# Kernel optimization log

Measured on AMD Instinct MI355X. Metric: run time of the kernel, lower is better.

## Reference

```python
import jax, jax.numpy as jnp
import numpy as np

N_NODES = 100000
N_EDGES = 1600000
N_GRAPHS = 1024
DIM_IN = 128
DIM_SELF = 16
BN_EPS = 1e-5


def _bn(x, gamma, beta):
    # training-mode BatchNorm1d over dim 0 (biased variance, as torch uses for normalization)
    m = jnp.mean(x, axis=0)
    v = jnp.mean((x - m) ** 2, axis=0)
    return gamma * (x - m) * jax.lax.rsqrt(v + BN_EPS) + beta


def _mlp(x, W1, b1, g, b, W2, b2):
    h = x @ W1 + b1
    h = jax.nn.relu(_bn(h, g, b))
    return h @ W2 + b2


def _gin(h, src, dst, W1, b1, g, b, W2, b2):
    # GINConv with eps=0: (1+eps)*h + sum over in-neighbors, then MLP
    agg = jax.ops.segment_sum(h[src], dst, num_segments=N_NODES)
    return _mlp(h + agg, W1, b1, g, b, W2, b2)


def setup_inputs() -> dict:
    key = jax.random.key(0)
    ks = jax.random.split(key, 16)

    def lin(k, fan_in, fan_out):
        bound = 1.0 / np.sqrt(fan_in)
        k1, k2 = jax.random.split(k)
        W = jax.random.uniform(k1, (fan_in, fan_out), jnp.float32, -bound, bound)
        b = jax.random.uniform(k2, (fan_out,), jnp.float32, -bound, bound)
        return W, b

    inp = {}
    inp['feat'] = jax.random.normal(ks[0], (N_NODES, DIM_IN), jnp.float32)
    inp['self_feat'] = jax.random.normal(ks[1], (N_GRAPHS, DIM_SELF), jnp.float32)
    inp['edge_src'] = jax.random.randint(ks[2], (N_EDGES,), 0, N_NODES, jnp.int32)
    inp['edge_dst'] = jax.random.randint(ks[3], (N_EDGES,), 0, N_NODES, jnp.int32)
    inp['node2graph'] = jnp.sort(jax.random.randint(ks[4], (N_NODES,), 0, N_GRAPHS, jnp.int32))

    inp['g1_W1'], inp['g1_b1'] = lin(ks[5], DIM_IN, 100)
    inp['g1_gamma'] = jnp.ones((100,), jnp.float32)
    inp['g1_beta'] = jnp.zeros((100,), jnp.float32)
    inp['g1_W2'], inp['g1_b2'] = lin(ks[6], 100, 100)

    inp['g2_W1'], inp['g2_b1'] = lin(ks[7], 100, 20)
    inp['g2_gamma'] = jnp.ones((20,), jnp.float32)
    inp['g2_beta'] = jnp.zeros((20,), jnp.float32)
    inp['g2_W2'], inp['g2_b2'] = lin(ks[8], 20, 20)

    inp['fc1_W'], inp['fc1_b'] = lin(ks[9], 20 * DIM_SELF, 32)
    inp['bn1_gamma'] = jnp.ones((32,), jnp.float32)
    inp['bn1_beta'] = jnp.zeros((32,), jnp.float32)
    inp['fc2_W'], inp['fc2_b'] = lin(ks[10], 32, 8)
    inp['bn2_gamma'] = jnp.ones((8,), jnp.float32)
    inp['bn2_beta'] = jnp.zeros((8,), jnp.float32)
    inp['fc3_W'], inp['fc3_b'] = lin(ks[11], 8, 1)
    return inp


def reference(feat, self_feat,
              g1_W1, g1_b1, g1_gamma, g1_beta, g1_W2, g1_b2,
              g2_W1, g2_b1, g2_gamma, g2_beta, g2_W2, g2_b2,
              fc1_W, fc1_b, bn1_gamma, bn1_beta,
              fc2_W, fc2_b, bn2_gamma, bn2_beta,
              fc3_W, fc3_b,
              edge_src, edge_dst, node2graph):
    h = _gin(feat, edge_src, edge_dst, g1_W1, g1_b1, g1_gamma, g1_beta, g1_W2, g1_b2)
    h = jax.nn.relu(h)
    h = _gin(h, edge_src, edge_dst, g2_W1, g2_b1, g2_gamma, g2_beta, g2_W2, g2_b2)
    h = jax.nn.relu(h)  # [N, 20]

    # dgl.mean_nodes: per-graph mean of node features
    sums = jax.ops.segment_sum(h, node2graph, num_segments=N_GRAPHS)  # [B, 20]
    cnts = jax.ops.segment_sum(jnp.ones((N_NODES,), h.dtype), node2graph, num_segments=N_GRAPHS)
    hg = sums / jnp.maximum(cnts, 1.0)[:, None]

    # kronecker fusion: bmm([B,20,1],[B,1,dim_self]) -> flatten
    kron = jnp.einsum('bi,bj->bij', hg, self_feat).reshape(N_GRAPHS, -1)  # [B, 20*dim_self]

    out = jax.nn.relu(_bn(kron @ fc1_W + fc1_b, bn1_gamma, bn1_beta))
    # dropout(0.3) is identity in eval mode
    out = jax.nn.relu(_bn(out @ fc2_W + fc2_b, bn2_gamma, bn2_beta))
    out = out @ fc3_W + fc3_b  # [B, dim_out]
    return out
```

## Files before the change

kernel.cpp:

```cpp
#include <hip/hip_runtime.h>

#define NN 100000
#define NE 1600000
#define NG 1024
#define DIN 128
#define D1 100
#define D2 20
#define DSELF 16
#define BN_EPS 1e-5f

#define NB 391
#define NBLK 782
#define EPB 2048
#define RAWCAP 5120
#define NAGG2 4000
#define NREP 64
#define APITCH 136

typedef unsigned int uint;
typedef unsigned short ushort;
typedef __attribute__((ext_vector_type(8))) short bfv8;
typedef __attribute__((ext_vector_type(4))) float fv4;

__device__ inline float bflo(uint x) { return __uint_as_float(x << 16); }
__device__ inline float bfhi(uint x) { return __uint_as_float(x & 0xffff0000u); }
__device__ inline uint packbf2(float a, float b) {
    uint ua = __float_as_uint(a), ub = __float_as_uint(b);
    ua += 0x7fffu + ((ua >> 16) & 1u);
    ub += 0x7fffu + ((ub >> 16) & 1u);
    return (ua >> 16) | (ub & 0xffff0000u);
}
__device__ inline ushort bfr(float x) {
    uint u = __float_as_uint(x);
    u += 0x7fffu + ((u >> 16) & 1u);
    return (ushort)(u >> 16);
}

__global__ __launch_bounds__(256) void k_gemm1(const float* __restrict__ feat,
                                               const float* __restrict__ W1,
                                               ushort* __restrict__ z1bf,
                                               float* __restrict__ pb1r) {
    __shared__ __align__(16) char smem[64 * APITCH * 2 + 112 * APITCH * 2];
    ushort* Al = (ushort*)smem;
    ushort* Bt = (ushort*)(smem + 64 * APITCH * 2);
    int t = threadIdx.x;
    if (blockIdx.x == 0) {
        for (int i = t; i < NREP * 200; i += 256) pb1r[i] = 0.f;
    }
    int row0 = blockIdx.x * 64;
#pragma unroll
    for (int i = 0; i < 8; i++) {
        int p = i * 256 + t;
        int r = p >> 5, cq = p & 31;
        int row = row0 + r; if (row >= NN) row = NN - 1;
        float4 v = *(const float4*)(feat + (size_t)row * DIN + cq * 4);
        ushort* dst = Al + r * APITCH + 4 * cq;
        dst[0] = bfr(v.x); dst[1] = bfr(v.y); dst[2] = bfr(v.z); dst[3] = bfr(v.w);
    }
    for (int p = t; p < 12800; p += 256) {
        int k = p / 100, n = p % 100;
        Bt[n * APITCH + k] = bfr(W1[p]);
    }
    __syncthreads();
    int w = __builtin_amdgcn_readfirstlane(t >> 6);
    int l = t & 63;
    int m16 = l & 15, quad = l >> 4;
    fv4 acc[7];
#pragma unroll
    for (int nt = 0; nt < 7; nt++) acc[nt] = (fv4){0.f, 0.f, 0.f, 0.f};
    const ushort* arow = Al + (w * 16 + m16) * APITCH;
#pragma unroll
    for (int kk = 0; kk < 4; kk++) {
        int kb = kk * 32 + quad * 8;
        bfv8 a = *(const bfv8*)(arow + kb);
#pragma unroll
        for (int nt = 0; nt < 7; nt++) {
            bfv8 b = *(const bfv8*)(Bt + (nt * 16 + m16) * APITCH + kb);
            acc[nt] = __builtin_amdgcn_mfma_f32_16x16x32_bf16(a, b, acc[nt], 0, 0, 0);
        }
    }
    __syncthreads();
    float* Ep = (float*)smem;
#pragma unroll
    for (int nt = 0; nt < 7; nt++) {
        int n = nt * 16 + m16;
        if (n < 100) {
#pragma unroll
            for (int rix = 0; rix < 4; rix++)
                Ep[(w * 16 + quad * 4 + rix) * 101 + n] = acc[nt][rix];
        }
    }
    __syncthreads();
#pragma unroll
    for (int i = 0; i < 13; i++) {
        int p = i * 256 + t;
        if (p < 3200) {
            int rr = p / 50, cc = 2 * (p % 50);
            int row = row0 + rr;
            if (row < NN) {
                float v0 = Ep[rr * 101 + cc], v1 = Ep[rr * 101 + cc + 1];
                *(uint*)(z1bf + (size_t)row * 128 + cc) = packbf2(v0, v1);
            }
        }
    }
}

__global__ __launch_bounds__(256) void k_csrA1(const int* __restrict__ dst,
                                               int* __restrict__ pbcount) {
    __shared__ int h[NB];
    int t = threadIdx.x, blk = blockIdx.x;
    for (int i = t; i < NB; i += 256) h[i] = 0;
    __syncthreads();
    int e0 = blk * EPB + t;
#pragma unroll
    for (int i = 0; i < 8; i++) {
        int e = e0 + i * 256;
        if (e < NE) atomicAdd(&h[dst[e] >> 8], 1);
    }
    __syncthreads();
    for (int i = t; i < NB; i += 256) pbcount[i * NBLK + blk] = h[i];
}

__global__ __launch_bounds__(1024) void k_csrS1(int* __restrict__ pbcount,
                                                int* __restrict__ btot) {
    __shared__ int s[1024];
    int t = threadIdx.x, b = blockIdx.x;
    int v = (t < NBLK) ? pbcount[b * NBLK + t] : 0;
    s[t] = v;
    __syncthreads();
    for (int off = 1; off < 1024; off <<= 1) {
        int x = (t >= off) ? s[t - off] : 0;
        __syncthreads();
        s[t] += x;
        __syncthreads();
    }
    if (t < NBLK) pbcount[b * NBLK + t] = s[t] - v;
    if (t == 1023) btot[b] = s[t];
}

__global__ __launch_bounds__(256) void k_csrA2(const int* __restrict__ src,
                                               const int* __restrict__ dst,
                                               const int* __restrict__ pbexcl,
                                               const int* __restrict__ btot,
                                               int* __restrict__ ebase_g,
                                               uint* __restrict__ gbuf) {
    __shared__ int cur[NB];
    __shared__ int sa[512], sb[512];
    int t = threadIdx.x, blk = blockIdx.x;
    int o0 = (t < NB) ? btot[t] : 0;
    int o1 = (t + 256 < NB) ? btot[t + 256] : 0;
    sa[t] = o0; sa[t + 256] = o1;
    __syncthreads();
    int* sp = sa; int* dp = sb;
    for (int off = 1; off < 512; off <<= 1) {
        dp[t] = sp[t] + ((t >= off) ? sp[t - off] : 0);
        int i2 = t + 256;
        dp[i2] = sp[i2] + ((i2 >= off) ? sp[i2 - off] : 0);
        __syncthreads();
        int* tmp = sp; sp = dp; dp = tmp;
    }
    if (t < NB)       cur[t]       = (sp[t] - o0) + pbexcl[t * NBLK + blk];
    if (t + 256 < NB) cur[t + 256] = (sp[t + 256] - o1) + pbexcl[(t + 256) * NBLK + blk];
    if (blk == 0) {
        if (t < NB)       ebase_g[t]       = sp[t] - o0;
        if (t + 256 < NB) ebase_g[t + 256] = sp[t + 256] - o1;
        if (t == 0)       ebase_g[NB]      = sp[NB - 1];
    }
    __syncthreads();
    int e0 = blk * EPB + t;
#pragma unroll
    for (int i = 0; i < 8; i++) {
        int e = e0 + i * 256;
        if (e < NE) {
            int d = dst[e];
            int b = d >> 8;
            int pos = atomicAdd(&cur[b], 1);
            gbuf[pos] = (uint)src[e] | ((uint)(d & 255) << 17);
        }
    }
}

__global__ __launch_bounds__(256) void k_csrB(const uint* __restrict__ gbuf,
                                              const int* __restrict__ ebase,
                                              int* __restrict__ deg,
                                              int* __restrict__ offs,
                                              int* __restrict__ srcS) {
    __shared__ uint raw[RAWCAP];
    __shared__ int srt[RAWCAP];
    __shared__ int pref[256], cur[256];
    int t = threadIdx.x, b = blockIdx.x;
    int e0 = ebase[b], e1 = ebase[b + 1];
    int cnt = e1 - e0; if (cnt > RAWCAP) cnt = RAWCAP;
    cur[t] = 0;
    for (int i = t; i < cnt; i += 256) raw[i] = gbuf[e0 + i];
    __syncthreads();
    for (int i = t; i < cnt; i += 256) atomicAdd(&cur[raw[i] >> 17], 1);
    __syncthreads();
    int v = cur[t];
    pref[t] = v;
    __syncthreads();
    for (int off = 1; off < 256; off <<= 1) {
        int x = (t >= off) ? pref[t - off] : 0;
        __syncthreads();
        pref[t] += x;
        __syncthreads();
    }
    int excl = pref[t] - v;
    int node = b * 256 + t;
    if (node < NN) { deg[node] = v; offs[node] = e0 + excl; }
    cur[t] = excl;
    __syncthreads();
    for (int i = t; i < cnt; i += 256) {
        uint p = raw[i];
        int lpos = atomicAdd(&cur[p >> 17], 1);
        srt[lpos] = (int)(p & 0x1FFFFu);
    }
    __syncthreads();
    for (int i = t; i < cnt; i += 256) srcS[e0 + i] = srt[i];
}

__global__ __launch_bounds__(256) void k_agg1(const ushort* __restrict__ z1bf,
                                              const int* __restrict__ offs,
                                              const int* __restrict__ deg,
                                              const int* __restrict__ srcS,
                                              ushort* __restrict__ u1b,
                                              float* __restrict__ pb1r) {
    int wv = __builtin_amdgcn_readfirstlane(threadIdx.x >> 6);
    int wid = blockIdx.x * 4 + wv;
    int l = threadIdx.x & 63;
    bool act = l < 50;
    const ushort* zc = z1bf + 2 * l;
    float S0 = 0.f, S1 = 0.f, Q0 = 0.f, Q1 = 0.f;
    int n0 = wid * 16;
    for (int k = 0; k < 16; k++) {
        int n = n0 + k;
        if (n >= NN) break;
        int d = deg[n], base = offs[n];
        float a0 = 0.f, a1 = 0.f, b0 = 0.f, b1 = 0.f;
        float c0 = 0.f, c1 = 0.f, e0 = 0.f, e1 = 0.f;
        int i = 0;
        for (; i + 8 <= d; i += 8) {
            int s0 = srcS[base + i],     s1 = srcS[base + i + 1];
            int s2 = srcS[base + i + 2], s3 = srcS[base + i + 3];
            int s4 = srcS[base + i + 4], s5 = srcS[base + i + 5];
            int s6 = srcS[base + i + 6], s7 = srcS[base + i + 7];
            if (act) {
                uint x0 = *(const uint*)(zc + (size_t)s0 * 128);
                uint x1 = *(const uint*)(zc + (size_t)s1 * 128);
                uint x2 = *(const uint*)(zc + (size_t)s2 * 128);
                uint x3 = *(const uint*)(zc + (size_t)s3 * 128);
                uint x4 = *(const uint*)(zc + (size_t)s4 * 128);
                uint x5 = *(const uint*)(zc + (size_t)s5 * 128);
                uint x6 = *(const uint*)(zc + (size_t)s6 * 128);
                uint x7 = *(const uint*)(zc + (size_t)s7 * 128);
                a0 += bflo(x0); a1 += bfhi(x0);
                b0 += bflo(x1); b1 += bfhi(x1);
                c0 += bflo(x2); c1 += bfhi(x2);
                e0 += bflo(x3); e1 += bfhi(x3);
                a0 += bflo(x4); a1 += bfhi(x4);
                b0 += bflo(x5); b1 += bfhi(x5);
                c0 += bflo(x6); c1 += bfhi(x6);
                e0 += bflo(x7); e1 += bfhi(x7);
            }
        }
        for (; i + 2 <= d; i += 2) {
            int s0 = srcS[base + i], s1 = srcS[base + i + 1];
            if (act) {
                uint x0 = *(const uint*)(zc + (size_t)s0 * 128);
                uint x1 = *(const uint*)(zc + (size_t)s1 * 128);
                a0 += bflo(x0); a1 += bfhi(x0);
                b0 += bflo(x1); b1 += bfhi(x1);
            }
        }
        if (i < d) {
            int s0 = srcS[base + i];
            if (act) {
                uint x0 = *(const uint*)(zc + (size_t)s0 * 128);
                a0 += bflo(x0); a1 += bfhi(x0);
            }
        }
        if (act) {
            uint xs = *(const uint*)(zc + (size_t)n * 128);
            float r0 = (a0 + b0) + (c0 + e0) + bflo(xs);
            float r1 = (a1 + b1) + (c1 + e1) + bfhi(xs);
            *(uint*)(u1b + (size_t)n * 100 + 2 * l) = packbf2(r0, r1);
            S0 += r0; S1 += r1;
            Q0 = fmaf(r0, r0, Q0); Q1 = fmaf(r1, r1, Q1);
        }
    }
    if (act) {
        float* rep = pb1r + (wid & (NREP - 1)) * 200;
        atomicAdd(&rep[2 * l], S0);
        atomicAdd(&rep[2 * l + 1], S1);
        atomicAdd(&rep[100 + 2 * l], Q0);
        atomicAdd(&rep[100 + 2 * l + 1], Q1);
    }
}

__global__ __launch_bounds__(256) void k_bnfin100(const float* __restrict__ pb1r,
                                                  const float* __restrict__ gamma,
                                                  const float* __restrict__ beta,
                                                  float* __restrict__ sc,
                                                  float* __restrict__ sh) {
    __shared__ float red[200];
    int t = threadIdx.x;
    if (t < 200) {
        float s = 0.f;
#pragma unroll 8
        for (int r = 0; r < NREP; r++) s += pb1r[r * 200 + t];
        red[t] = s;
    }
    __syncthreads();
    if (t < 100) {
        float S = red[t], Q = red[100 + t];
        float mean = S * (1.f / NN);
        float var = Q * (1.f / NN) - mean * mean;
        float inv = rsqrtf(var + BN_EPS);
        float s = gamma[t] * inv;
        sc[t] = s;
        sh[t] = beta[t] - mean * s;
    }
}

__global__ __launch_bounds__(256) void k_m2(const ushort* __restrict__ u1b,
                                            const float* __restrict__ sc,
                                            const float* __restrict__ sh,
                                            const float* __restrict__ W2,
                                            const float* __restrict__ b2,
                                            const float* __restrict__ W1p,
                                            ushort* __restrict__ z2bf,
                                            float* __restrict__ pb2r) {
    __shared__ float Xs[100 * 65];
    int t = threadIdx.x;
    if (blockIdx.x == 0) {
        for (int i = t; i < NREP * 40; i += 256) pb2r[i] = 0.f;
    }
    int row0 = blockIdx.x * 64;
#pragma unroll
    for (int i = 0; i < 13; i++) {
        int p = i * 256 + t;
        if (p < 3200) {
            int r = p / 50, c = 2 * (p % 50);
            int row = row0 + r; if (row >= NN) row = NN - 1;
            uint x = *(const uint*)(u1b + (size_t)row * 100 + c);
            Xs[c * 65 + r] = fmaxf(bflo(x) * sc[c] + sh[c], 0.f);
            Xs[(c + 1) * 65 + r] = fmaxf(bfhi(x) * sc[c + 1] + sh[c + 1], 0.f);
        }
    }
    __syncthreads();
    int cg = __builtin_amdgcn_readfirstlane(t >> 6);
    int r = t & 63;
    int j0 = cg * 25;
    float H[25];
#pragma unroll
    for (int m = 0; m < 25; m++) H[m] = 0.f;
    for (int k = 0; k < D1; k++) {
        float a = Xs[k * 65 + r];
        const float* wr = W2 + k * D1 + j0;
#pragma unroll
        for (int m = 0; m < 25; m++) H[m] = fmaf(a, wr[m], H[m]);
    }
#pragma unroll
    for (int m = 0; m < 25; m++) H[m] = fmaxf(H[m] + b2[j0 + m], 0.f);
    float pz[20];
#pragma unroll
    for (int c = 0; c < 20; c++) pz[c] = 0.f;
#pragma unroll
    for (int m = 0; m < 25; m++) {
        const float* wp = W1p + (j0 + m) * D2;
#pragma unroll
        for (int c = 0; c < 20; c++) pz[c] = fmaf(H[m], wp[c], pz[c]);
    }
    __syncthreads();
    float* red = Xs;
#pragma unroll
    for (int c = 0; c < 20; c++) red[t * 20 + c] = pz[c];
    __syncthreads();
#pragma unroll
    for (int i = 0; i < 3; i++) {
        int p = i * 256 + t;
        if (p < 640) {
            int rr = p / 10, c2 = 2 * (p % 10);
            int row = row0 + rr;
            if (row < NN) {
                float v0 = red[rr * 20 + c2] + red[(64 + rr) * 20 + c2] +
                           red[(128 + rr) * 20 + c2] + red[(192 + rr) * 20 + c2];
                float v1 = red[rr * 20 + c2 + 1] + red[(64 + rr) * 20 + c2 + 1] +
                           red[(128 + rr) * 20 + c2 + 1] + red[(192 + rr) * 20 + c2 + 1];
                *(uint*)(z2bf + (size_t)row * 32 + c2) = packbf2(v0, v1);
            }
        }
    }
}

__global__ __launch_bounds__(256) void k_agg2(const ushort* __restrict__ z2bf,
                                              const int* __restrict__ offs,
                                              const int* __restrict__ deg,
                                              const int* __restrict__ srcS,
                                              float* __restrict__ u2,
                                              float* __restrict__ pb2r) {
    __shared__ float ls[500], lq[500];
    int t = threadIdx.x;
    int n = blockIdx.x * 25 + t / 10;
    int c2 = 2 * (t % 10);
    float r0 = 0.f, r1 = 0.f;
    if (t < 250 && n < NN) {
        int d = deg[n], base = offs[n];
        const ushort* zc = z2bf + c2;
        float a0 = 0.f, a1 = 0.f, b0 = 0.f, b1 = 0.f;
        int i = 0;
        for (; i + 2 <= d; i += 2) {
            uint x0 = *(const uint*)(zc + (size_t)srcS[base + i] * 32);
            uint x1 = *(const uint*)(zc + (size_t)srcS[base + i + 1] * 32);
            a0 += bflo(x0); a1 += bfhi(x0);
            b0 += bflo(x1); b1 += bfhi(x1);
        }
        if (i < d) {
            uint x0 = *(const uint*)(zc + (size_t)srcS[base + i] * 32);
            a0 += bflo(x0); a1 += bfhi(x0);
        }
        uint xs = *(const uint*)(zc + (size_t)n * 32);
        r0 = a0 + b0 + bflo(xs);
        r1 = a1 + b1 + bfhi(xs);
        *(float2*)(u2 + (size_t)n * D2 + c2) = make_float2(r0, r1);
    }
    if (t < 250) {
        int idx = (t / 10) * 20 + c2;
        ls[idx] = r0;     lq[idx] = r0 * r0;
        ls[idx + 1] = r1; lq[idx + 1] = r1 * r1;
    }
    __syncthreads();
    if (t < 20) {
        float S = 0.f, Q = 0.f;
#pragma unroll
        for (int j = 0; j < 25; j++) { S += ls[j * 20 + t]; Q += lq[j * 20 + t]; }
        int rep = (blockIdx.x & (NREP - 1)) * 40;
        atomicAdd(&pb2r[rep + t], S);
        atomicAdd(&pb2r[rep + 20 + t], Q);
    }
}

__global__ __launch_bounds__(64) void k_bnfin20(const float* __restrict__ pb2r,
                                                const float* __restrict__ gamma,
                                                const float* __restrict__ beta,
                                                float* __restrict__ sc,
                                                float* __restrict__ sh) {
    __shared__ float red[40];
    int t = threadIdx.x;
    if (t < 40) {
        float s = 0.f;
#pragma unroll 8
        for (int r = 0; r < NREP; r++) s += pb2r[r * 40 + t];
        red[t] = s;
    }
    __syncthreads();
    if (t < 20) {
        float S = red[t], Q = red[20 + t];
        float mean = S * (1.f / NN);
        float var = Q * (1.f / NN) - mean * mean;
        float inv = rsqrtf(var + BN_EPS);
        float s = gamma[t] * inv;
        sc[t] = s;
        sh[t] = beta[t] - mean * s;
    }
}

__global__ __launch_bounds__(256) void k_m3(const float* __restrict__ u2,
                                            const float* __restrict__ sc,
                                            const float* __restrict__ sh,
                                            const float* __restrict__ W2p,
                                            const float* __restrict__ b2p,
                                            float* __restrict__ h2) {
    int row = blockIdx.x * 256 + threadIdx.x;
    if (row >= NN) return;
    float ya[20];
    const float4* up = (const float4*)(u2 + (size_t)row * D2);
#pragma unroll
    for (int i = 0; i < 5; i++) {
        float4 v = up[i];
        float4 S = *(const float4*)(sc + 4 * i);
        float4 H = *(const float4*)(sh + 4 * i);
        ya[4 * i + 0] = fmaxf(v.x * S.x + H.x, 0.f);
        ya[4 * i + 1] = fmaxf(v.y * S.y + H.y, 0.f);
        ya[4 * i + 2] = fmaxf(v.z * S.z + H.z, 0.f);
        ya[4 * i + 3] = fmaxf(v.w * S.w + H.w, 0.f);
    }
    float hrow[D2];
#pragma unroll
    for (int j = 0; j < D2; j++) {
        float h = b2p[j];
#pragma unroll
        for (int k = 0; k < D2; k++) h = fmaf(ya[k], W2p[k * D2 + j], h);
        hrow[j] = fmaxf(h, 0.f);
    }
    float* hr = h2 + (size_t)row * D2;
#pragma unroll
    for (int c = 0; c < D2; c += 4) {
        float4 o; o.x = hrow[c]; o.y = hrow[c + 1]; o.z = hrow[c + 2]; o.w = hrow[c + 3];
        *(float4*)(hr + c) = o;
    }
}

__global__ __launch_bounds__(256) void k_pool(const float* __restrict__ h2,
                                              const int* __restrict__ n2g,
                                              float* __restrict__ hg) {
    int wq = __builtin_amdgcn_readfirstlane(threadIdx.x >> 6);
    int l = threadIdx.x & 63;
    int g = blockIdx.x * 4 + wq;
    if (g >= NG) return;
    int lo = 0, hi = NN;
    while (lo < hi) { int mid = (lo + hi) >> 1; if (n2g[mid] < g) lo = mid + 1; else hi = mid; }
    int s0 = lo;
    hi = NN;
    while (lo < hi) { int mid = (lo + hi) >> 1; if (n2g[mid] < g + 1) lo = mid + 1; else hi = mid; }
    int s1 = lo;
    float a = 0.f;
    if (l < 60) {
        int rg = l / 20, c = l % 20;
        for (int n = s0 + rg; n < s1; n += 3) a += h2[(size_t)n * D2 + c];
    }
    float v1 = __shfl(a, l + 20, 64);
    float v2 = __shfl(a, l + 40, 64);
    if (l < 20) {
        float cnt = (float)(s1 - s0);
        hg[g * D2 + l] = (a + v1 + v2) / fmaxf(cnt, 1.f);
    }
}

__global__ void k_head1(const float* __restrict__ hg, const float* __restrict__ sf,
                        const float* __restrict__ fc1W, float* __restrict__ a1) {
    int b = blockIdx.x * 8 + threadIdx.x / 32;
    int c = threadIdx.x % 32;
    if (b >= NG) return;
    const float* hgb = hg + b * D2;
    const float* sfb = sf + b * DSELF;
    float acc = 0.f;
    for (int i = 0; i < D2; i++) {
        float hi = hgb[i];
#pragma unroll
        for (int j = 0; j < DSELF; j++)
            acc += hi * sfb[j] * fc1W[(i * DSELF + j) * 32 + c];
    }
    a1[b * 32 + c] = acc;
}

__global__ __launch_bounds__(1024) void k_head2(
    const float* __restrict__ a1, const float* __restrict__ g1,
    const float* __restrict__ be1, const float* __restrict__ fc2W,
    const float* __restrict__ g2, const float* __restrict__ be2,
    const float* __restrict__ fc3W, const float* __restrict__ fc3b,
    float* __restrict__ out) {
    int t = threadIdx.x;
    int lane = t & 63, w = t >> 6;
    __shared__ float s1[16][32], s2[16][32];
    __shared__ float sc[32], sh[32], sc2[8], sh2[8];
    float x[32];
    const float4* ap = (const float4*)(a1 + t * 32);
#pragma unroll
    for (int i = 0; i < 8; i++) {
        float4 v = ap[i];
        x[4 * i] = v.x; x[4 * i + 1] = v.y; x[4 * i + 2] = v.z; x[4 * i + 3] = v.w;
    }
#pragma unroll
    for (int c = 0; c < 32; c++) {
        float v = x[c], q = v * v;
        for (int o = 32; o > 0; o >>= 1) {
            v += __shfl_down(v, o, 64);
            q += __shfl_down(q, o, 64);
        }
        if (lane == 0) { s1[w][c] = v; s2[w][c] = q; }
    }
    __syncthreads();
    if (t < 32) {
        float s = 0.f, q = 0.f;
        for (int ww = 0; ww < 16; ww++) { s += s1[ww][t]; q += s2[ww][t]; }
        float mean = s * (1.f / NG);
        float var = q * (1.f / NG) - mean * mean;
        float inv = rsqrtf(var + BN_EPS);
        float scl = g1[t] * inv;
        sc[t] = scl;
        sh[t] = be1[t] - mean * scl;
    }
    __syncthreads();
#pragma unroll
    for (int c = 0; c < 32; c++) x[c] = fmaxf(x[c] * sc[c] + sh[c], 0.f);
    float y[8];
#pragma unroll
    for (int p = 0; p < 8; p++) {
        float a = 0.f;
#pragma unroll
        for (int c = 0; c < 32; c++) a += x[c] * fc2W[c * 8 + p];
        y[p] = a;
    }
    __syncthreads();
#pragma unroll
    for (int p = 0; p < 8; p++) {
        float v = y[p], q = v * v;
        for (int o = 32; o > 0; o >>= 1) {
            v += __shfl_down(v, o, 64);
            q += __shfl_down(q, o, 64);
        }
        if (lane == 0) { s1[w][p] = v; s2[w][p] = q; }
    }
    __syncthreads();
    if (t < 8) {
        float s = 0.f, q = 0.f;
        for (int ww = 0; ww < 16; ww++) { s += s1[ww][t]; q += s2[ww][t]; }
        float mean = s * (1.f / NG);
        float var = q * (1.f / NG) - mean * mean;
        float inv = rsqrtf(var + BN_EPS);
        float scl = g2[t] * inv;
        sc2[t] = scl;
        sh2[t] = be2[t] - mean * scl;
    }
    __syncthreads();
    float o = fc3b[0];
#pragma unroll
    for (int p = 0; p < 8; p++) {
        float yy = fmaxf(y[p] * sc2[p] + sh2[p], 0.f);
        o += yy * fc3W[p];
    }
    out[t] = o;
}

extern "C" void kernel_launch(void* const* d_in, const int* in_sizes, int n_in,
                              void* d_out, int out_size, void* d_ws, size_t ws_size,
                              hipStream_t stream) {
    const float* feat    = (const float*)d_in[0];
    const float* sf      = (const float*)d_in[1];
    const int*   esrc    = (const int*)d_in[2];
    const int*   edst    = (const int*)d_in[3];
    const int*   n2g     = (const int*)d_in[4];
    const float* g1W1    = (const float*)d_in[5];
    const float* g1gam   = (const float*)d_in[7];
    const float* g1bet   = (const float*)d_in[8];
    const float* g1W2    = (const float*)d_in[9];
    const float* g1b2    = (const float*)d_in[10];
    const float* g2W1    = (const float*)d_in[11];
    const float* g2gam   = (const float*)d_in[13];
    const float* g2bet   = (const float*)d_in[14];
    const float* g2W2    = (const float*)d_in[15];
    const float* g2b2    = (const float*)d_in[16];
    const float* fc1W    = (const float*)d_in[17];
    const float* hbn1g   = (const float*)d_in[19];
    const float* hbn1b   = (const float*)d_in[20];
    const float* fc2W    = (const float*)d_in[21];
    const float* hbn2g   = (const float*)d_in[23];
    const float* hbn2b   = (const float*)d_in[24];
    const float* fc3W    = (const float*)d_in[25];
    const float* fc3b    = (const float*)d_in[26];
    float* out = (float*)d_out;

    char* w = (char*)d_ws;
    size_t off = 0;
    auto alloc = [&](size_t bytes) -> char* {
        char* p = w + off;
        off += (bytes + 15) & ~(size_t)15;
        return p;
    };
    char* regA = alloc((size_t)NN * 128 * 2);
    ushort* z1bf = (ushort*)regA;
    ushort* z2bf = (ushort*)regA;
    float*  u2   = (float*)(regA + 6400000);
    float*  h2   = (float*)(regA + 14400000);
    ushort* u1b  = (ushort*)alloc((size_t)NN * 100 * 2);
    int*   pbcnt = (int*)alloc((size_t)NB * NBLK * 4);
    int*   btot  = (int*)alloc(NB * 4);
    int*   ebase = (int*)alloc((NB + 1) * 4);
    uint*  gbuf  = (uint*)alloc((size_t)NE * 4);
    int*   deg   = (int*)alloc(NN * 4);
    int*   offs  = (int*)alloc(NN * 4);
    int*   srcS  = (int*)alloc((size_t)NE * 4);
    float* pb1r  = (float*)alloc((size_t)NREP * 200 * 4);
    float* pb2r  = (float*)alloc((size_t)NREP * 40 * 4);
    float* sc1   = (float*)alloc(D1 * 4);
    float* sh1   = (float*)alloc(D1 * 4);
    float* sc2   = (float*)alloc(D2 * 4);
    float* sh2   = (float*)alloc(D2 * 4);
    float* hg    = (float*)alloc(NG * D2 * 4);
    float* a1    = (float*)alloc(NG * 32 * 4);
    (void)in_sizes; (void)n_in; (void)out_size; (void)ws_size;

    k_gemm1<<<(NN + 63) / 64, 256, 0, stream>>>(feat, g1W1, z1bf, pb1r);

    k_csrA1<<<NBLK, 256, 0, stream>>>(edst, pbcnt);
    k_csrS1<<<NB, 1024, 0, stream>>>(pbcnt, btot);
    k_csrA2<<<NBLK, 256, 0, stream>>>(esrc, edst, pbcnt, btot, ebase, gbuf);
    k_csrB<<<NB, 256, 0, stream>>>(gbuf, ebase, deg, offs, srcS);

    k_agg1<<<1563, 256, 0, stream>>>(z1bf, offs, deg, srcS, u1b, pb1r);
    k_bnfin100<<<1, 256, 0, stream>>>(pb1r, g1gam, g1bet, sc1, sh1);
    k_m2<<<(NN + 63) / 64, 256, 0, stream>>>(u1b, sc1, sh1, g1W2, g1b2, g2W1, z2bf, pb2r);

    k_agg2<<<NAGG2, 256, 0, stream>>>(z2bf, offs, deg, srcS, u2, pb2r);
    k_bnfin20<<<1, 64, 0, stream>>>(pb2r, g2gam, g2bet, sc2, sh2);
    k_m3<<<(NN + 255) / 256, 256, 0, stream>>>(u2, sc2, sh2, g2W2, g2b2, h2);

    k_pool<<<(NG + 3) / 4, 256, 0, stream>>>(h2, n2g, hg);
    k_head1<<<NG / 8, 256, 0, stream>>>(hg, sf, fc1W, a1);
    k_head2<<<1, 1024, 0, stream>>>(a1, hbn1g, hbn1b, fc2W, hbn2g, hbn2b, fc3W, fc3b, out);
}
```

Measured before the change: 439.9 us.

## Fuse final MLP with mean pooling and rebalance agg1 work per wave

The second GIN's output MLP now does the per-graph segment sum directly. It reduces runs of equal graph ids in shared memory and atomically adds them into a zeroed hgsum buffer, so the h2 intermediate and the separate pool kernel go away. The division by node count moves into the head kernel, which now binary-searches node2graph for each graph's count. Separately, agg1 gives each wave 4 nodes instead of 16 and launches four times as many blocks to balance load. It also reduces BN statistics within the block in shared memory before one atomic per feature, which cuts global atomics but adds a block barrier.

```diff
diff --git a/kernel.cpp b/kernel.cpp
--- a/kernel.cpp
+++ b/kernel.cpp
@@ -225,16 +225,17 @@
                                               const int* __restrict__ srcS,
                                               ushort* __restrict__ u1b,
                                               float* __restrict__ pb1r) {
-    int wv = __builtin_amdgcn_readfirstlane(threadIdx.x >> 6);
-    int wid = blockIdx.x * 4 + wv;
-    int l = threadIdx.x & 63;
+    __shared__ float part[4][200];
+    int t = threadIdx.x;
+    int wv = __builtin_amdgcn_readfirstlane(t >> 6);
+    int l = t & 63;
     bool act = l < 50;
     const ushort* zc = z1bf + 2 * l;
     float S0 = 0.f, S1 = 0.f, Q0 = 0.f, Q1 = 0.f;
-    int n0 = wid * 16;
-    for (int k = 0; k < 16; k++) {
+    int n0 = blockIdx.x * 16 + wv * 4;
+#pragma unroll 1
+    for (int k = 0; k < 4; k++) {
         int n = n0 + k;
-        if (n >= NN) break;
         int d = deg[n], base = offs[n];
         float a0 = 0.f, a1 = 0.f, b0 = 0.f, b1 = 0.f;
         float c0 = 0.f, c1 = 0.f, e0 = 0.f, e1 = 0.f;
@@ -289,11 +290,13 @@
         }
     }
     if (act) {
-        float* rep = pb1r + (wid & (NREP - 1)) * 200;
-        atomicAdd(&rep[2 * l], S0);
-        atomicAdd(&rep[2 * l + 1], S1);
-        atomicAdd(&rep[100 + 2 * l], Q0);
-        atomicAdd(&rep[100 + 2 * l + 1], Q1);
+        part[wv][2 * l] = S0;        part[wv][2 * l + 1] = S1;
+        part[wv][100 + 2 * l] = Q0;  part[wv][100 + 2 * l + 1] = Q1;
+    }
+    __syncthreads();
+    if (t < 200) {
+        float s = part[0][t] + part[1][t] + part[2][t] + part[3][t];
+        atomicAdd(&pb1r[(blockIdx.x & (NREP - 1)) * 200 + t], s);
     }
 }
 
@@ -329,11 +332,13 @@
                                             const float* __restrict__ b2,
                                             const float* __restrict__ W1p,
                                             ushort* __restrict__ z2bf,
-                                            float* __restrict__ pb2r) {
+                                            float* __restrict__ pb2r,
+                                            float* __restrict__ hgsum) {
     __shared__ float Xs[100 * 65];
     int t = threadIdx.x;
     if (blockIdx.x == 0) {
         for (int i = t; i < NREP * 40; i += 256) pb2r[i] = 0.f;
+        for (int i = t; i < NG * D2; i += 256) hgsum[i] = 0.f;
     }
     int row0 = blockIdx.x * 64;
 #pragma unroll
@@ -465,81 +470,84 @@
     }
 }
 
-__global__ __launch_bounds__(256) void k_m3(const float* __restrict__ u2,
-                                            const float* __restrict__ sc,
-                                            const float* __restrict__ sh,
-                                            const float* __restrict__ W2p,
-                                            const float* __restrict__ b2p,
-                                            float* __restrict__ h2) {
-    int row = blockIdx.x * 256 + threadIdx.x;
-    if (row >= NN) return;
-    float ya[20];
-    const float4* up = (const float4*)(u2 + (size_t)row * D2);
-#pragma unroll
-    for (int i = 0; i < 5; i++) {
-        float4 v = up[i];
-        float4 S = *(const float4*)(sc + 4 * i);
-        float4 H = *(const float4*)(sh + 4 * i);
-        ya[4 * i + 0] = fmaxf(v.x * S.x + H.x, 0.f);
-        ya[4 * i + 1] = fmaxf(v.y * S.y + H.y, 0.f);
-        ya[4 * i + 2] = fmaxf(v.z * S.z + H.z, 0.f);
-        ya[4 * i + 3] = fmaxf(v.w * S.w + H.w, 0.f);
-    }
+__global__ __launch_bounds__(256) void k_m3p(const float* __restrict__ u2,
+                                             const float* __restrict__ sc,
+                                             const float* __restrict__ sh,
+                                             const float* __restrict__ W2p,
+                                             const float* __restrict__ b2p,
+                                             const int* __restrict__ n2g,
+                                             float* __restrict__ hgsum) {
+    __shared__ float X[256][21];
+    __shared__ int gl[256];
+    int t = threadIdx.x;
+    int row = blockIdx.x * 256 + t;
+    bool valid = row < NN;
+    gl[t] = valid ? n2g[row] : -1;
     float hrow[D2];
-#pragma unroll
-    for (int j = 0; j < D2; j++) {
-        float h = b2p[j];
-#pragma unroll
-        for (int k = 0; k < D2; k++) h = fmaf(ya[k], W2p[k * D2 + j], h);
-        hrow[j] = fmaxf(h, 0.f);
-    }
-    float* hr = h2 + (size_t)row * D2;
-#pragma unroll
-    for (int c = 0; c < D2; c += 4) {
-        float4 o; o.x = hrow[c]; o.y = hrow[c + 1]; o.z = hrow[c + 2]; o.w = hrow[c + 3];
-        *(float4*)(hr + c) = o;
-    }
-}
-
-__global__ __launch_bounds__(256) void k_pool(const float* __restrict__ h2,
-                                              const int* __restrict__ n2g,
-                                              float* __restrict__ hg) {
-    int wq = __builtin_amdgcn_readfirstlane(threadIdx.x >> 6);
-    int l = threadIdx.x & 63;
-    int g = blockIdx.x * 4 + wq;
-    if (g >= NG) return;
-    int lo = 0, hi = NN;
-    while (lo < hi) { int mid = (lo + hi) >> 1; if (n2g[mid] < g) lo = mid + 1; else hi = mid; }
-    int s0 = lo;
-    hi = NN;
-    while (lo < hi) { int mid = (lo + hi) >> 1; if (n2g[mid] < g + 1) lo = mid + 1; else hi = mid; }
-    int s1 = lo;
-    float a = 0.f;
-    if (l < 60) {
-        int rg = l / 20, c = l % 20;
-        for (int n = s0 + rg; n < s1; n += 3) a += h2[(size_t)n * D2 + c];
-    }
-    float v1 = __shfl(a, l + 20, 64);
-    float v2 = __shfl(a, l + 40, 64);
-    if (l < 20) {
-        float cnt = (float)(s1 - s0);
-        hg[g * D2 + l] = (a + v1 + v2) / fmaxf(cnt, 1.f);
-    }
-}
-
-__global__ void k_head1(const float* __restrict__ hg, const float* __restrict__ sf,
+    if (valid) {
+        float ya[20];
+        const float4* up = (const float4*)(u2 + (size_t)row * D2);
+#pragma unroll
+        for (int i = 0; i < 5; i++) {
+            float4 v = up[i];
+            float4 S = *(const float4*)(sc + 4 * i);
+            float4 H = *(const float4*)(sh + 4 * i);
+            ya[4 * i + 0] = fmaxf(v.x * S.x + H.x, 0.f);
+            ya[4 * i + 1] = fmaxf(v.y * S.y + H.y, 0.f);
+            ya[4 * i + 2] = fmaxf(v.z * S.z + H.z, 0.f);
+            ya[4 * i + 3] = fmaxf(v.w * S.w + H.w, 0.f);
+        }
+#pragma unroll
+        for (int j = 0; j < D2; j++) {
+            float h = b2p[j];
+#pragma unroll
+            for (int k = 0; k < D2; k++) h = fmaf(ya[k], W2p[k * D2 + j], h);
+            hrow[j] = fmaxf(h, 0.f);
+        }
+#pragma unroll
+        for (int j = 0; j < D2; j++) X[t][j] = hrow[j];
+    } else {
+#pragma unroll
+        for (int j = 0; j < D2; j++) X[t][j] = 0.f;
+    }
+    __syncthreads();
+    if (t < 160) {
+        int seg = t / 20, j = t % 20;
+        int i0 = seg * 32, i1 = i0 + 32;
+        int gprev = -2;
+        float acc = 0.f;
+        for (int i = i0; i < i1; i++) {
+            int gi = gl[i];
+            if (gi != gprev) {
+                if (gprev >= 0) atomicAdd(&hgsum[gprev * D2 + j], acc);
+                gprev = gi; acc = 0.f;
+            }
+            acc += X[i][j];
+        }
+        if (gprev >= 0) atomicAdd(&hgsum[gprev * D2 + j], acc);
+    }
+}
+
+__global__ void k_head1(const float* __restrict__ hgsum, const int* __restrict__ n2g,
+                        const float* __restrict__ sf,
                         const float* __restrict__ fc1W, float* __restrict__ a1) {
     int b = blockIdx.x * 8 + threadIdx.x / 32;
     int c = threadIdx.x % 32;
     if (b >= NG) return;
-    const float* hgb = hg + b * D2;
+    int lo = 0, hi2 = NN;
+    while (lo < hi2) { int mid = (lo + hi2) >> 1; if (n2g[mid] < b) lo = mid + 1; else hi2 = mid; }
+    int s0 = lo;
+    hi2 = NN;
+    while (lo < hi2) { int mid = (lo + hi2) >> 1; if (n2g[mid] < b + 1) lo = mid + 1; else hi2 = mid; }
+    float rc = 1.f / fmaxf((float)(lo - s0), 1.f);
+    const float* hgb = hgsum + b * D2;
     const float* sfb = sf + b * DSELF;
     float acc = 0.f;
     for (int i = 0; i < D2; i++) {
-        float hi = hgb[i];
+        float hv = hgb[i] * rc;
 #pragma unroll
         for (int j = 0; j < DSELF; j++)
-            acc += hi * sfb[j] * fc1W[(i * DSELF + j) * 32 + c];
+            acc += hv * sfb[j] * fc1W[(i * DSELF + j) * 32 + c];
     }
     a1[b * 32 + c] = acc;
 }
@@ -662,7 +670,6 @@
     ushort* z1bf = (ushort*)regA;
     ushort* z2bf = (ushort*)regA;
     float*  u2   = (float*)(regA + 6400000);
-    float*  h2   = (float*)(regA + 14400000);
     ushort* u1b  = (ushort*)alloc((size_t)NN * 100 * 2);
     int*   pbcnt = (int*)alloc((size_t)NB * NBLK * 4);
     int*   btot  = (int*)alloc(NB * 4);
@@ -677,7 +684,7 @@
     float* sh1   = (float*)alloc(D1 * 4);
     float* sc2   = (float*)alloc(D2 * 4);
     float* sh2   = (float*)alloc(D2 * 4);
-    float* hg    = (float*)alloc(NG * D2 * 4);
+    float* hgsum = (float*)alloc((size_t)NG * D2 * 4);
     float* a1    = (float*)alloc(NG * 32 * 4);
     (void)in_sizes; (void)n_in; (void)out_size; (void)ws_size;
 
@@ -688,15 +695,14 @@
     k_csrA2<<<NBLK, 256, 0, stream>>>(esrc, edst, pbcnt, btot, ebase, gbuf);
     k_csrB<<<NB, 256, 0, stream>>>(gbuf, ebase, deg, offs, srcS);
 
-    k_agg1<<<1563, 256, 0, stream>>>(z1bf, offs, deg, srcS, u1b, pb1r);
+    k_agg1<<<NN / 16, 256, 0, stream>>>(z1bf, offs, deg, srcS, u1b, pb1r);
     k_bnfin100<<<1, 256, 0, stream>>>(pb1r, g1gam, g1bet, sc1, sh1);
-    k_m2<<<(NN + 63) / 64, 256, 0, stream>>>(u1b, sc1, sh1, g1W2, g1b2, g2W1, z2bf, pb2r);
+    k_m2<<<(NN + 63) / 64, 256, 0, stream>>>(u1b, sc1, sh1, g1W2, g1b2, g2W1, z2bf, pb2r, hgsum);
 
     k_agg2<<<NAGG2, 256, 0, stream>>>(z2bf, offs, deg, srcS, u2, pb2r);
     k_bnfin20<<<1, 64, 0, stream>>>(pb2r, g2gam, g2bet, sc2, sh2);
-    k_m3<<<(NN + 255) / 256, 256, 0, stream>>>(u2, sc2, sh2, g2W2, g2b2, h2);
-
-    k_pool<<<(NG + 3) / 4, 256, 0, stream>>>(h2, n2g, hg);
-    k_head1<<<NG / 8, 256, 0, stream>>>(hg, sf, fc1W, a1);
+    k_m3p<<<(NN + 255) / 256, 256, 0, stream>>>(u2, sc2, sh2, g2W2, g2b2, n2g, hgsum);
+
+    k_head1<<<NG / 8, 256, 0, stream>>>(hgsum, n2g, sf, fc1W, a1);
     k_head2<<<1, 1024, 0, stream>>>(a1, hbn1g, hbn1b, fc2W, hbn2g, hbn2b, fc3W, fc3b, out);
 }
```

Result: faster. 410.9 us (-6.6%).
